# Kernel optimization log

Hardware: AMD Instinct MI355X
Metric: run time of the kernel (lower is better)

Reference implementation:

```python
import jax, jax.numpy as jnp
import numpy as np

B, J, D = 512, 22, 3
HIDDEN = 512
OUT = J * D          # 66, flattened frame size
NCLS = 12
LENGTH = 64


def setup_inputs() -> dict:
    key = jax.random.key(0)
    ks = jax.random.split(key, 12)
    s = 0.05
    return {
        "inputs": jax.random.normal(ks[0], (B, J, D), dtype=jnp.float32),
        "labels": jax.random.randint(ks[1], (B,), 0, NCLS),
        "length": LENGTH,
        # LSTMCell params (torch layout: W_ih [4H, in], W_hh [4H, H], gate order i,f,g,o)
        "W_ih": jax.random.normal(ks[2], (4 * HIDDEN, OUT + NCLS), dtype=jnp.float32) * s,
        "W_hh": jax.random.normal(ks[3], (4 * HIDDEN, HIDDEN), dtype=jnp.float32) * s,
        "b_ih": jax.random.normal(ks[4], (4 * HIDDEN,), dtype=jnp.float32) * s,
        "b_hh": jax.random.normal(ks[5], (4 * HIDDEN,), dtype=jnp.float32) * s,
        # fc: hidden -> output
        "W_fc": jax.random.normal(ks[6], (OUT, HIDDEN), dtype=jnp.float32) * s,
        "b_fc": jax.random.normal(ks[7], (OUT,), dtype=jnp.float32) * s,
        # fc_inh / fc_inc: output -> hidden (initial state projections)
        "W_inh": jax.random.normal(ks[8], (HIDDEN, OUT), dtype=jnp.float32) * s,
        "b_inh": jax.random.normal(ks[9], (HIDDEN,), dtype=jnp.float32) * s,
        "W_inc": jax.random.normal(ks[10], (HIDDEN, OUT), dtype=jnp.float32) * s,
        "b_inc": jax.random.normal(ks[11], (HIDDEN,), dtype=jnp.float32) * s,
    }


def reference(inputs, labels, length, W_ih, W_hh, b_ih, b_hh, W_fc, b_fc,
              W_inh, b_inh, W_inc, b_inc):
    b, j, d = inputs.shape
    enc = jax.nn.one_hot(labels, NCLS, dtype=inputs.dtype)      # [B, NCLS]
    frame0 = inputs.reshape(b, j * d)                            # [B, OUT]
    h0 = frame0 @ W_inh.T + b_inh                                # [B, H]
    c0 = frame0 @ W_inc.T + b_inc                                # [B, H]
    frame = jnp.concatenate([frame0, enc], axis=-1)              # [B, OUT+NCLS]

    def step(carry, _):
        h, c, fr = carry
        gates = fr @ W_ih.T + b_ih + h @ W_hh.T + b_hh           # [B, 4H]
        i, f, g, o = jnp.split(gates, 4, axis=-1)                # torch gate order
        c_new = jax.nn.sigmoid(f) * c + jax.nn.sigmoid(i) * jnp.tanh(g)
        h_new = jax.nn.sigmoid(o) * jnp.tanh(c_new)
        out = h_new @ W_fc.T + b_fc                              # [B, OUT]
        fr_new = jnp.concatenate([out, enc], axis=-1)
        return (h_new, c_new, fr_new), out

    _, outs = jax.lax.scan(step, (h0, c0, frame), None, length=length)  # [L, B, OUT]
    return jnp.transpose(outs, (1, 0, 2)).reshape(b, length, j, d)
```

## Files before the change

### kernel.cpp

```cpp
#include <hip/hip_runtime.h>

#define OUTD 66
#define INW  78
#define FH   2048
#define LEN  64

typedef short bf16x8 __attribute__((ext_vector_type(8)));
typedef float f32x4  __attribute__((ext_vector_type(4)));
typedef unsigned int u32x4 __attribute__((ext_vector_type(4)));

__device__ __forceinline__ float bf2f(unsigned short u) {
  union { unsigned int i; float f; } v; v.i = ((unsigned int)u) << 16; return v.f;
}
__device__ __forceinline__ unsigned short f2bf(float f) {
  union { float f; unsigned int i; } v; v.f = f;
  unsigned int u = v.i;
  return (unsigned short)((u + 0x7fffu + ((u >> 16) & 1u)) >> 16);
}
__device__ __forceinline__ float sigm(float x) { return 1.f / (1.f + __expf(-x)); }
__device__ __forceinline__ float tanh_f(float x) { return 2.f / (1.f + __expf(-2.f * x)) - 1.f; }

__device__ __forceinline__ unsigned int atom_or_ret(unsigned int* p, unsigned int d) {
  unsigned int r;
  asm volatile("global_atomic_or %0, %1, %2, off sc0\n\ts_waitcnt vmcnt(0)"
               : "=&v"(r) : "v"(p), "v"(d) : "memory");
  return r;
}
__device__ __forceinline__ void atom_or(unsigned int* p, unsigned int d) {
  asm volatile("global_atomic_or %0, %1, off" :: "v"(p), "v"(d) : "memory");
}

__global__ __launch_bounds__(256) void k_initA(
    const float* __restrict__ W_hh, const float* __restrict__ W_ih,
    const float* __restrict__ W_fc, const float* __restrict__ b_ih,
    const float* __restrict__ b_hh, const float* __restrict__ b_fc,
    const float* __restrict__ inp, const float* __restrict__ W_inh,
    const float* __restrict__ b_inh, const float* __restrict__ W_inc,
    const float* __restrict__ b_inc,
    unsigned short* __restrict__ Weff, float* __restrict__ bias_eff,
    unsigned short* __restrict__ hbuf, float* __restrict__ c0,
    unsigned short* __restrict__ Wfc16, unsigned int* __restrict__ flags,
    unsigned int* __restrict__ flagsL)
{
  int tid = threadIdx.x, bid = blockIdx.x;
  if (bid < 256) {
    int nb = bid;
    int k = tid * 2;
    float acc[8][2];
    #pragma unroll
    for (int r = 0; r < 8; ++r) {
      int n = nb * 8 + r;
      acc[r][0] = W_hh[n * 512 + k];
      acc[r][1] = W_hh[n * 512 + k + 1];
    }
    for (int m = 0; m < OUTD; ++m) {
      float w0 = W_fc[m * 512 + k];
      float w1 = W_fc[m * 512 + k + 1];
      #pragma unroll
      for (int r = 0; r < 8; ++r) {
        float wih = W_ih[(nb * 8 + r) * INW + m];
        acc[r][0] += wih * w0;
        acc[r][1] += wih * w1;
      }
    }
    #pragma unroll
    for (int r = 0; r < 8; ++r) {
      int n = nb * 8 + r;
      unsigned int pack = (unsigned int)f2bf(acc[r][0]) | ((unsigned int)f2bf(acc[r][1]) << 16);
      *(unsigned int*)(Weff + n * 512 + k) = pack;
    }
    if (tid < 8) {
      int n = nb * 8 + tid;
      float a = b_ih[n] + b_hh[n];
      for (int m = 0; m < OUTD; ++m) a += b_fc[m] * W_ih[n * INW + m];
      bias_eff[n] = a;
    }
    if (nb == 0) {
      for (int i = tid; i < 512 * 16; i += 256) flags[i] = 0;
      for (int i = tid; i < 256 * 16; i += 256) flagsL[i] = 0;
    }
  } else {
    int nb = bid - 256;
    for (int r = 0; r < 2; ++r) {
      int b = nb * 2 + r;
      for (int half = 0; half < 2; ++half) {
        int c = tid + half * 256;
        float ha = b_inh[c], ca = b_inc[c];
        for (int m = 0; m < OUTD; ++m) {
          float f = inp[b * OUTD + m];
          ha += f * W_inh[c * OUTD + m];
          ca += f * W_inc[c * OUTD + m];
        }
        hbuf[((b >> 6) * 32 + (c >> 4)) * 1024 + (b & 63) * 16 + (c & 15)] = f2bf(ha);
        c0[b * 512 + c] = ca;
      }
    }
    if (nb == 0) {
      for (int i = tid; i < OUTD * 512; i += 256) Wfc16[i] = f2bf(W_fc[i]);
    }
  }
}

__global__ __launch_bounds__(128) void k_init2a(
    const float* __restrict__ inp, const unsigned short* __restrict__ hbuf,
    const float* __restrict__ W_fc, const float* __restrict__ b_fc,
    float* __restrict__ d0)
{
  int b = blockIdx.x, m = threadIdx.x;
  if (m >= OUTD) return;
  const unsigned short* hb = hbuf + (b >> 6) * 32768 + (b & 63) * 16;
  const float* wrow = W_fc + m * 512;
  float acc = 0.f;
  for (int k = 0; k < 512; ++k)
    acc += bf2f(hb[(k >> 4) * 1024 + (k & 15)]) * wrow[k];
  d0[b * OUTD + m] = inp[b * OUTD + m] - (acc + b_fc[m]);
}

__global__ __launch_bounds__(256) void k_init2b(
    const float* __restrict__ d0, const float* __restrict__ W_ih,
    float* __restrict__ corr0)
{
  __shared__ float ds[4][OUTD];
  int tid = threadIdx.x, b0 = blockIdx.x * 4;
  for (int i = tid; i < 4 * OUTD; i += 256) ds[i / OUTD][i % OUTD] = d0[b0 * OUTD + i];
  __syncthreads();
  for (int n = tid; n < FH; n += 256) {
    float a0 = 0, a1 = 0, a2 = 0, a3 = 0;
    const float* wr = W_ih + n * INW;
    for (int m = 0; m < OUTD; ++m) {
      float w = wr[m];
      a0 += ds[0][m] * w; a1 += ds[1][m] * w; a2 += ds[2][m] * w; a3 += ds[3][m] * w;
    }
    corr0[(b0 + 0) * FH + n] = a0;
    corr0[(b0 + 1) * FH + n] = a1;
    corr0[(b0 + 2) * FH + n] = a2;
    corr0[(b0 + 3) * FH + n] = a3;
  }
}

__global__ __launch_bounds__(256, 1) void k_main(
    const unsigned short* __restrict__ Weff, const float* __restrict__ bias_eff,
    unsigned short* __restrict__ hbuf, const float* __restrict__ c0,
    const float* __restrict__ corr0, const float* __restrict__ W_ih,
    const int* __restrict__ labels, const unsigned short* __restrict__ Wfc16,
    const float* __restrict__ b_fc, float* __restrict__ out,
    unsigned int* __restrict__ flags, unsigned int* __restrict__ flagsL)
{
  __shared__ __align__(16) unsigned short h_lds[64 * 512];

  int tid = threadIdx.x, bid = blockIdx.x;
  int w = tid >> 6, lane = tid & 63;
  int lc = lane & 15, kg = lane >> 4;
  unsigned int* xmap = flags + 4096;
  unsigned int* decp = flags + 4088;
  unsigned int* maskW = flagsL;

  unsigned int xcd;
  asm volatile("s_getreg_b32 %0, hwreg(HW_REG_XCC_ID)" : "=s"(xcd));
  if (tid == 0)
    __hip_atomic_store(&xmap[bid * 16], xcd + 1u, __ATOMIC_RELAXED, __HIP_MEMORY_SCOPE_AGENT);

  if (bid == 0 && w == 0) {
    int okA = 1, okB = 1;
    #pragma unroll
    for (int i = 0; i < 4; ++i) {
      int b = lane + i * 64;
      unsigned int v, ra, rb;
      const unsigned int* xp = &xmap[b * 16];
      for (;;) { v = __hip_atomic_load(xp, __ATOMIC_RELAXED, __HIP_MEMORY_SCOPE_AGENT);
                 if (v) break; __builtin_amdgcn_s_sleep(1); }
      const unsigned int* pa = &xmap[(b & 7) * 16];
      for (;;) { ra = __hip_atomic_load(pa, __ATOMIC_RELAXED, __HIP_MEMORY_SCOPE_AGENT);
                 if (ra) break; __builtin_amdgcn_s_sleep(1); }
      const unsigned int* pb = &xmap[((b >> 5) << 5) * 16];
      for (;;) { rb = __hip_atomic_load(pb, __ATOMIC_RELAXED, __HIP_MEMORY_SCOPE_AGENT);
                 if (rb) break; __builtin_amdgcn_s_sleep(1); }
      okA &= (v == ra); okB &= (v == rb);
    }
    okA = __all(okA); okB = __all(okB);
    if (lane == 0) {
      unsigned int d = okA ? 1u : (okB ? 2u : 3u);
      __hip_atomic_store(decp, d, __ATOMIC_RELAXED, __HIP_MEMORY_SCOPE_AGENT);
    }
  }
  if (tid == 0) {
    unsigned int dd;
    for (;;) { dd = __hip_atomic_load(decp, __ATOMIC_RELAXED, __HIP_MEMORY_SCOPE_AGENT);
               if (dd) break; __builtin_amdgcn_s_sleep(1); }
    h_lds[0] = (unsigned short)dd;
  }
  __syncthreads();
  unsigned int dmode = h_lds[0];
  __syncthreads();

  int fast, mt, jt;
  if (dmode == 1u)      { fast = 1; mt = bid & 7;  jt = bid >> 3; }
  else if (dmode == 2u) { fast = 1; mt = bid >> 5; jt = bid & 31; }
  else                  { fast = 0; mt = bid & 7;  jt = bid >> 3; }

  int row0 = mt * 64, j0 = jt * 16;
  int hx0 = (w >> 1) * 8;
  int xloc = lc & 7;
  int G = lc >> 3;
  int hcol = j0 + hx0 + xloc;
  int rw0 = (w & 1) * 32;

  int sA = xloc;
  int tA16 = ((kg ^ sA) & 3) << 4;
  int ue64 = ((sA >> 2) & 1) << 6;
  int PA0 = (rw0 + lc) * 1024 + tA16 + ue64;
  int PA1 = PA0 + 16 * 1024;
  int PF  = (w * 16 + lc) * 1024 + tA16 + ue64;

  bf16x8 Bfrag[16][2];
  #pragma unroll
  for (int cg = 0; cg < 2; ++cg) {
    int n = (cg * 2 + G) * 512 + hcol;
    const unsigned short* p = Weff + n * 512 + kg * 8;
    #pragma unroll
    for (int i = 0; i < 16; ++i) Bfrag[i][cg] = *(const bf16x8*)(p + i * 32);
  }

  bf16x8 Wf[16];
  float fcb = 0.f;
  {
    int n = j0 + lc;
    if (jt < 5 && n < OUTD) {
      const unsigned short* p = Wfc16 + n * 512 + kg * 8;
      #pragma unroll
      for (int i = 0; i < 16; ++i) Wf[i] = *(const bf16x8*)(p + i * 32);
      fcb = b_fc[n];
    } else {
      bf16x8 z8 = {0, 0, 0, 0, 0, 0, 0, 0};
      #pragma unroll
      for (int i = 0; i < 16; ++i) Wf[i] = z8;
    }
  }

  int qsel = G * 2;
  float lt[4][4], creg[4];
  #pragma unroll
  for (int idx = 0; idx < 4; ++idx) {
    int rloc = rw0 + (idx >> 1) * 16 + kg * 4 + qsel + (idx & 1);
    int grow = row0 + rloc;
    int lab = labels[grow];
    #pragma unroll
    for (int gt = 0; gt < 4; ++gt) {
      int n = gt * 512 + hcol;
      lt[gt][idx] = bias_eff[n] + W_ih[n * INW + OUTD + lab];
    }
    creg[idx] = c0[grow * 512 + hcol];
  }

  const f32x4 z = {0.f, 0.f, 0.f, 0.f};
  unsigned int* myflag = &flags[(mt * 32 + jt) * 16];

  {
    const unsigned short* hsrc = hbuf + mt * 32768;
    #pragma unroll
    for (int i = 0; i < 16; ++i) {
      int n = tid + i * 256;
      int c = n >> 7, q = n & 127;
      int r = q >> 1, u = q & 1, g = c * 2 + u;
      *(u32x4*)(h_lds + r * 512 + ((g ^ (r & 7)) << 3)) =
          *(const u32x4*)(hsrc + n * 8);
    }
  }
  __syncthreads();

  for (int s = 0; s < LEN; ++s) {
    f32x4 acc00 = z, acc01 = z, acc10 = z, acc11 = z;
    #pragma unroll
    for (int i = 0; i < 16; ++i) {
      bf16x8 a0 = *(const bf16x8*)((const char*)h_lds + (PA0 ^ (i << 6)));
      bf16x8 a1 = *(const bf16x8*)((const char*)h_lds + (PA1 ^ (i << 6)));
      acc00 = __builtin_amdgcn_mfma_f32_16x16x32_bf16(a0, Bfrag[i][0], acc00, 0, 0, 0);
      acc10 = __builtin_amdgcn_mfma_f32_16x16x32_bf16(a1, Bfrag[i][0], acc10, 0, 0, 0);
      acc01 = __builtin_amdgcn_mfma_f32_16x16x32_bf16(a0, Bfrag[i][1], acc01, 0, 0, 0);
      acc11 = __builtin_amdgcn_mfma_f32_16x16x32_bf16(a1, Bfrag[i][1], acc11, 0, 0, 0);
    }

    f32x4 sh00, sh01, sh10, sh11;
    #pragma unroll
    for (int j = 0; j < 4; ++j) {
      sh00[j] = __shfl_xor(acc00[j], 8);
      sh01[j] = __shfl_xor(acc01[j], 8);
      sh10[j] = __shfl_xor(acc10[j], 8);
      sh11[j] = __shfl_xor(acc11[j], 8);
    }

    unsigned short hval[4];
    #pragma unroll
    for (int idx = 0; idx < 4; ++idx) {
      int jj = idx & 1, hh = idx >> 1;
      int qo = qsel + jj;
      float xi, xf, xg, xo;
      if (hh == 0) {
        xi = (G ? sh00[qo] : acc00[qo]);
        xf = (G ? acc00[qo] : sh00[qo]);
        xg = (G ? sh01[qo] : acc01[qo]);
        xo = (G ? acc01[qo] : sh01[qo]);
      } else {
        xi = (G ? sh10[qo] : acc10[qo]);
        xf = (G ? acc10[qo] : sh10[qo]);
        xg = (G ? sh11[qo] : acc11[qo]);
        xo = (G ? acc11[qo] : sh11[qo]);
      }
      xi += lt[0][idx]; xf += lt[1][idx]; xg += lt[2][idx]; xo += lt[3][idx];
      if (s == 0) {
        int rloc = rw0 + hh * 16 + kg * 4 + qo;
        const float* cr = corr0 + (long)(row0 + rloc) * FH + hcol;
        xi += cr[0]; xf += cr[512]; xg += cr[1024]; xo += cr[1536];
      }
      float cn = sigm(xf) * creg[idx] + sigm(xi) * tanh_f(xg);
      creg[idx] = cn;
      hval[idx] = f2bf(sigm(xo) * tanh_f(cn));
    }

    unsigned int pkS[2]; int rlS[2];
    {
      unsigned int* hdst32 = (unsigned int*)(hbuf + ((s + 1) & 1) * 262144);
      int base32 = (mt * 32 + jt) * 512;
      int ceL = (hx0 >> 1) + (xloc >> 1);
      int odd = xloc & 1;
      int np = 0;
      #pragma unroll
      for (int idx = 0; idx < 4; ++idx) {
        unsigned int mine = hval[idx];
        unsigned int part = (unsigned int)__shfl_xor((int)mine, 1);
        unsigned int p = odd ? (part | (mine << 16)) : (mine | (part << 16));
        if ((idx >> 1) == odd) {
          int rloc = rw0 + (idx >> 1) * 16 + kg * 4 + qsel + (idx & 1);
          pkS[np] = p; rlS[np] = rloc; ++np;
        }
      }
      if (fast) {
        hdst32[base32 + rlS[0] * 8 + ceL] = pkS[0];
        hdst32[base32 + rlS[1] * 8 + ceL] = pkS[1];
      } else {
        __hip_atomic_store(&hdst32[base32 + rlS[0] * 8 + ceL], pkS[0],
                           __ATOMIC_RELAXED, __HIP_MEMORY_SCOPE_AGENT);
        __hip_atomic_store(&hdst32[base32 + rlS[1] * 8 + ceL], pkS[1],
                           __ATOMIC_RELAXED, __HIP_MEMORY_SCOPE_AGENT);
      }
    }

    __builtin_amdgcn_s_waitcnt(0);
    __syncthreads();
    if (tid == 0) {
      if (fast)
        atom_or(&maskW[(mt * 4 + (jt >> 3)) * 64 + s], 1u << (jt & 7));
      __hip_atomic_store(myflag, (unsigned int)(s + 1),
                         __ATOMIC_RELAXED, __HIP_MEMORY_SCOPE_AGENT);
    }

    f32x4 fa = z;
    int dofc = (jt < 5) & (s >= 1);
    if (dofc) {
      #pragma unroll
      for (int i = 0; i < 16; ++i) {
        bf16x8 a = *(const bf16x8*)((const char*)h_lds + (PF ^ (i << 6)));
        fa = __builtin_amdgcn_mfma_f32_16x16x32_bf16(a, Wf[i], fa, 0, 0, 0);
      }
    }
    __syncthreads();

    {
      int gS = jt * 2 + (w >> 1);
      unsigned int* l32 = (unsigned int*)h_lds;
      #pragma unroll
      for (int t = 0; t < 2; ++t) {
        int rl = rlS[t];
        l32[rl * 256 + ((gS ^ (rl & 7)) << 2) + (xloc >> 1)] = pkS[t];
      }
    }

    if (s < LEN - 1 || jt < 5) {
      const unsigned short* hbC = hbuf + ((s + 1) & 1) * 262144 + mt * 32768;
      unsigned int mydone = (w == (jt >> 3)) ? (1u << (jt & 7)) : 0u;
      const unsigned int* fA = flags + (mt * 32 + w * 8 + (lane & 7)) * 16;
      unsigned int* mg = &maskW[(mt * 4 + w) * 64 + s];
      int agentMode = !fast;
      int spins = 0;
      while (mydone != 0xffu) {
        unsigned int avail;
        if (!agentMode) {
          unsigned int v = 0;
          if (lane == 0) v = atom_or_ret(mg, 0u);
          avail = (unsigned int)__shfl((int)v, 0);
          if (++spins > 1024) agentMode = 1;
        } else {
          unsigned int fv = __hip_atomic_load(fA, __ATOMIC_RELAXED, __HIP_MEMORY_SCOPE_AGENT);
          avail = (unsigned int)__ballot((int)(fv >= (unsigned int)(s + 1))) & 0xffu;
        }
        unsigned int todo = avail & ~mydone;
        if (!todo) { __builtin_amdgcn_s_sleep(1); continue; }

        if (agentMode)
          __builtin_amdgcn_fence(__ATOMIC_ACQUIRE, "agent");
        else
          asm volatile("buffer_inv\n\ts_waitcnt vmcnt(0)" ::: "memory");

        u32x4 ta[8], tb[8];
        #pragma unroll
        for (int i = 0; i < 8; ++i) {
          if ((todo >> i) & 1u) {
            const unsigned short* cp = hbC + (w * 8 + i) * 1024 + lane * 8;
            ta[i] = *(const u32x4*)cp;
            tb[i] = *(const u32x4*)(cp + 512);
          }
        }
        int r0_ = lane >> 1, u = lane & 1, r1_ = 32 + r0_;
        #pragma unroll
        for (int i = 0; i < 8; ++i) {
          if ((todo >> i) & 1u) {
            int c2 = (w * 8 + i) * 2 + u;
            *(u32x4*)(h_lds + r0_ * 512 + ((c2 ^ (r0_ & 7)) << 3)) = ta[i];
            *(u32x4*)(h_lds + r1_ * 512 + ((c2 ^ (r1_ & 7)) << 3)) = tb[i];
          }
        }
        mydone |= todo;
      }
    }

    if (dofc) {
      int c = j0 + lc;
      if (c < OUTD) {
        #pragma unroll
        for (int q = 0; q < 4; ++q) {
          int b = row0 + w * 16 + kg * 4 + q;
          out[((long)b * 64 + (s - 1)) * OUTD + c] = fa[q] + fcb;
        }
      }
    }
    __syncthreads();
  }

  if (jt < 5) {
    f32x4 fa = z;
    #pragma unroll
    for (int i = 0; i < 16; ++i) {
      bf16x8 a = *(const bf16x8*)((const char*)h_lds + (PF ^ (i << 6)));
      fa = __builtin_amdgcn_mfma_f32_16x16x32_bf16(a, Wf[i], fa, 0, 0, 0);
    }
    int c = j0 + lc;
    if (c < OUTD) {
      #pragma unroll
      for (int q = 0; q < 4; ++q) {
        int b = row0 + w * 16 + kg * 4 + q;
        out[((long)b * 64 + 63) * OUTD + c] = fa[q] + fcb;
      }
    }
  }
}

extern "C" void kernel_launch(void* const* d_in, const int* in_sizes, int n_in,
                              void* d_out, int out_size, void* d_ws, size_t ws_size,
                              hipStream_t stream) {
  (void)in_sizes; (void)n_in; (void)out_size; (void)ws_size;
  const float* inp   = (const float*)d_in[0];
  const int*   labels= (const int*)d_in[1];
  const float* W_ih  = (const float*)d_in[3];
  const float* W_hh  = (const float*)d_in[4];
  const float* b_ih  = (const float*)d_in[5];
  const float* b_hh  = (const float*)d_in[6];
  const float* W_fc  = (const float*)d_in[7];
  const float* b_fc  = (const float*)d_in[8];
  const float* W_inh = (const float*)d_in[9];
  const float* b_inh = (const float*)d_in[10];
  const float* W_inc = (const float*)d_in[11];
  const float* b_inc = (const float*)d_in[12];

  char* ws = (char*)d_ws;
  unsigned short* Weff = (unsigned short*)(ws + 0);
  float* bias_eff      = (float*)(ws + 2097152);
  unsigned short* hbuf = (unsigned short*)(ws + 2105344);
  float* c0            = (float*)(ws + 3153920);
  float* corr0         = (float*)(ws + 4202496);
  float* d0            = (float*)(ws + 8396800);
  unsigned int* flags  = (unsigned int*)(ws + 8531968);
  unsigned short* Wfc16= (unsigned short*)(ws + 8564736);
  unsigned int* flagsL = (unsigned int*)(ws + 8632320);

  k_initA<<<512, 256, 0, stream>>>(W_hh, W_ih, W_fc, b_ih, b_hh, b_fc,
                                   inp, W_inh, b_inh, W_inc, b_inc,
                                   Weff, bias_eff, hbuf, c0, Wfc16, flags, flagsL);
  k_init2a<<<512, 128, 0, stream>>>(inp, hbuf, W_fc, b_fc, d0);
  k_init2b<<<128, 256, 0, stream>>>(d0, W_ih, corr0);

  k_main<<<256, 256, 0, stream>>>(Weff, bias_eff, hbuf, c0, corr0, W_ih, labels,
                                  Wfc16, b_fc, (float*)d_out, flags, flagsL);
}
```

Baseline: 450.8 us.

## Split persistent LSTM kernel into 512 blocks with 32-row batch tiles

Halves the batch rows per block from 64 to 32 and doubles the persistent grid to 512 blocks with two blocks per CU, rearranging the hidden-state buffer layout, flag strides and XCD mapping to match. Each block now does half the MFMA work per step, and the FC output store is deferred into the next step to overlap with compute. This gives more parallelism per step but doubles the number of blocks taking part in the cross-block flag synchronisation, and it relies on all 512 blocks being co-resident.

```diff
diff --git a/kernel.cpp b/kernel.cpp
--- a/kernel.cpp
+++ b/kernel.cpp
@@ -91,7 +91,7 @@
           ha += f * W_inh[c * OUTD + m];
           ca += f * W_inc[c * OUTD + m];
         }
-        hbuf[((b >> 6) * 32 + (c >> 4)) * 1024 + (b & 63) * 16 + (c & 15)] = f2bf(ha);
+        hbuf[((b >> 5) * 32 + (c >> 4)) * 512 + (b & 31) * 16 + (c & 15)] = f2bf(ha);
         c0[b * 512 + c] = ca;
       }
     }
@@ -108,11 +108,11 @@
 {
   int b = blockIdx.x, m = threadIdx.x;
   if (m >= OUTD) return;
-  const unsigned short* hb = hbuf + (b >> 6) * 32768 + (b & 63) * 16;
+  const unsigned short* hb = hbuf + (b >> 5) * 16384 + (b & 31) * 16;
   const float* wrow = W_fc + m * 512;
   float acc = 0.f;
   for (int k = 0; k < 512; ++k)
-    acc += bf2f(hb[(k >> 4) * 1024 + (k & 15)]) * wrow[k];
+    acc += bf2f(hb[(k >> 4) * 512 + (k & 15)]) * wrow[k];
   d0[b * OUTD + m] = inp[b * OUTD + m] - (acc + b_fc[m]);
 }
 
@@ -138,7 +138,7 @@
   }
 }
 
-__global__ __launch_bounds__(256, 1) void k_main(
+__global__ __launch_bounds__(256, 2) void k_main(
     const unsigned short* __restrict__ Weff, const float* __restrict__ bias_eff,
     unsigned short* __restrict__ hbuf, const float* __restrict__ c0,
     const float* __restrict__ corr0, const float* __restrict__ W_ih,
@@ -146,33 +146,33 @@
     const float* __restrict__ b_fc, float* __restrict__ out,
     unsigned int* __restrict__ flags, unsigned int* __restrict__ flagsL)
 {
-  __shared__ __align__(16) unsigned short h_lds[64 * 512];
+  __shared__ __align__(16) unsigned short h_lds[32 * 512];
 
   int tid = threadIdx.x, bid = blockIdx.x;
   int w = tid >> 6, lane = tid & 63;
   int lc = lane & 15, kg = lane >> 4;
-  unsigned int* xmap = flags + 4096;
-  unsigned int* decp = flags + 4088;
+  unsigned int* xmap = flags + 4608;
+  unsigned int* decp = flags + 4100;
   unsigned int* maskW = flagsL;
 
   unsigned int xcd;
   asm volatile("s_getreg_b32 %0, hwreg(HW_REG_XCC_ID)" : "=s"(xcd));
   if (tid == 0)
-    __hip_atomic_store(&xmap[bid * 16], xcd + 1u, __ATOMIC_RELAXED, __HIP_MEMORY_SCOPE_AGENT);
+    __hip_atomic_store(&xmap[bid * 4], xcd + 1u, __ATOMIC_RELAXED, __HIP_MEMORY_SCOPE_AGENT);
 
   if (bid == 0 && w == 0) {
     int okA = 1, okB = 1;
     #pragma unroll
-    for (int i = 0; i < 4; ++i) {
+    for (int i = 0; i < 8; ++i) {
       int b = lane + i * 64;
       unsigned int v, ra, rb;
-      const unsigned int* xp = &xmap[b * 16];
+      const unsigned int* xp = &xmap[b * 4];
       for (;;) { v = __hip_atomic_load(xp, __ATOMIC_RELAXED, __HIP_MEMORY_SCOPE_AGENT);
                  if (v) break; __builtin_amdgcn_s_sleep(1); }
-      const unsigned int* pa = &xmap[(b & 7) * 16];
+      const unsigned int* pa = &xmap[(b & 15) * 4];
       for (;;) { ra = __hip_atomic_load(pa, __ATOMIC_RELAXED, __HIP_MEMORY_SCOPE_AGENT);
                  if (ra) break; __builtin_amdgcn_s_sleep(1); }
-      const unsigned int* pb = &xmap[((b >> 5) << 5) * 16];
+      const unsigned int* pb = &xmap[((b >> 5) << 5) * 4];
       for (;;) { rb = __hip_atomic_load(pb, __ATOMIC_RELAXED, __HIP_MEMORY_SCOPE_AGENT);
                  if (rb) break; __builtin_amdgcn_s_sleep(1); }
       okA &= (v == ra); okB &= (v == rb);
@@ -194,23 +194,22 @@
   __syncthreads();
 
   int fast, mt, jt;
-  if (dmode == 1u)      { fast = 1; mt = bid & 7;  jt = bid >> 3; }
-  else if (dmode == 2u) { fast = 1; mt = bid >> 5; jt = bid & 31; }
-  else                  { fast = 0; mt = bid & 7;  jt = bid >> 3; }
-
-  int row0 = mt * 64, j0 = jt * 16;
+  if (dmode == 1u)      { fast = 1; mt = bid & 15;  jt = bid >> 4; }
+  else if (dmode == 2u) { fast = 1; mt = bid >> 5;  jt = bid & 31; }
+  else                  { fast = 0; mt = bid & 15;  jt = bid >> 4; }
+
+  int row0 = mt * 32, j0 = jt * 16;
   int hx0 = (w >> 1) * 8;
   int xloc = lc & 7;
   int G = lc >> 3;
   int hcol = j0 + hx0 + xloc;
-  int rw0 = (w & 1) * 32;
+  int rw0 = (w & 1) * 16;
 
   int sA = xloc;
   int tA16 = ((kg ^ sA) & 3) << 4;
   int ue64 = ((sA >> 2) & 1) << 6;
   int PA0 = (rw0 + lc) * 1024 + tA16 + ue64;
-  int PA1 = PA0 + 16 * 1024;
-  int PF  = (w * 16 + lc) * 1024 + tA16 + ue64;
+  int PF  = ((w & 1) * 16 + lc) * 1024 + tA16 + ue64;
 
   bf16x8 Bfrag[16][2];
   #pragma unroll
@@ -225,7 +224,7 @@
   float fcb = 0.f;
   {
     int n = j0 + lc;
-    if (jt < 5 && n < OUTD) {
+    if (jt < 5 && w < 2 && n < OUTD) {
       const unsigned short* p = Wfc16 + n * 512 + kg * 8;
       #pragma unroll
       for (int i = 0; i < 16; ++i) Wf[i] = *(const bf16x8*)(p + i * 32);
@@ -238,10 +237,10 @@
   }
 
   int qsel = G * 2;
-  float lt[4][4], creg[4];
+  float lt[4][2], creg[2];
   #pragma unroll
-  for (int idx = 0; idx < 4; ++idx) {
-    int rloc = rw0 + (idx >> 1) * 16 + kg * 4 + qsel + (idx & 1);
+  for (int idx = 0; idx < 2; ++idx) {
+    int rloc = rw0 + kg * 4 + qsel + idx;
     int grow = row0 + rloc;
     int lab = labels[grow];
     #pragma unroll
@@ -253,14 +252,14 @@
   }
 
   const f32x4 z = {0.f, 0.f, 0.f, 0.f};
-  unsigned int* myflag = &flags[(mt * 32 + jt) * 16];
+  unsigned int* myflag = &flags[(mt * 32 + jt) * 8];
 
   {
-    const unsigned short* hsrc = hbuf + mt * 32768;
-    #pragma unroll
-    for (int i = 0; i < 16; ++i) {
+    const unsigned short* hsrc = hbuf + mt * 16384;
+    #pragma unroll
+    for (int i = 0; i < 8; ++i) {
       int n = tid + i * 256;
-      int c = n >> 7, q = n & 127;
+      int c = n >> 6, q = n & 63;
       int r = q >> 1, u = q & 1, g = c * 2 + u;
       *(u32x4*)(h_lds + r * 512 + ((g ^ (r & 7)) << 3)) =
           *(const u32x4*)(hsrc + n * 8);
@@ -268,47 +267,48 @@
   }
   __syncthreads();
 
+  f32x4 faP = z; int havP = 0, colP = 0;
+  int dofcW = (jt < 5) & (w < 2);
+
   for (int s = 0; s < LEN; ++s) {
-    f32x4 acc00 = z, acc01 = z, acc10 = z, acc11 = z;
+    if (havP) {
+      int c = j0 + lc;
+      if (c < OUTD) {
+        #pragma unroll
+        for (int q = 0; q < 4; ++q) {
+          int b = row0 + (w & 1) * 16 + kg * 4 + q;
+          out[((long)b * 64 + colP) * OUTD + c] = faP[q] + fcb;
+        }
+      }
+      havP = 0;
+    }
+
+    f32x4 acc00 = z, acc01 = z;
     #pragma unroll
     for (int i = 0; i < 16; ++i) {
       bf16x8 a0 = *(const bf16x8*)((const char*)h_lds + (PA0 ^ (i << 6)));
-      bf16x8 a1 = *(const bf16x8*)((const char*)h_lds + (PA1 ^ (i << 6)));
       acc00 = __builtin_amdgcn_mfma_f32_16x16x32_bf16(a0, Bfrag[i][0], acc00, 0, 0, 0);
-      acc10 = __builtin_amdgcn_mfma_f32_16x16x32_bf16(a1, Bfrag[i][0], acc10, 0, 0, 0);
       acc01 = __builtin_amdgcn_mfma_f32_16x16x32_bf16(a0, Bfrag[i][1], acc01, 0, 0, 0);
-      acc11 = __builtin_amdgcn_mfma_f32_16x16x32_bf16(a1, Bfrag[i][1], acc11, 0, 0, 0);
-    }
-
-    f32x4 sh00, sh01, sh10, sh11;
+    }
+
+    f32x4 sh00, sh01;
     #pragma unroll
     for (int j = 0; j < 4; ++j) {
       sh00[j] = __shfl_xor(acc00[j], 8);
       sh01[j] = __shfl_xor(acc01[j], 8);
-      sh10[j] = __shfl_xor(acc10[j], 8);
-      sh11[j] = __shfl_xor(acc11[j], 8);
-    }
-
-    unsigned short hval[4];
-    #pragma unroll
-    for (int idx = 0; idx < 4; ++idx) {
-      int jj = idx & 1, hh = idx >> 1;
-      int qo = qsel + jj;
-      float xi, xf, xg, xo;
-      if (hh == 0) {
-        xi = (G ? sh00[qo] : acc00[qo]);
-        xf = (G ? acc00[qo] : sh00[qo]);
-        xg = (G ? sh01[qo] : acc01[qo]);
-        xo = (G ? acc01[qo] : sh01[qo]);
-      } else {
-        xi = (G ? sh10[qo] : acc10[qo]);
-        xf = (G ? acc10[qo] : sh10[qo]);
-        xg = (G ? sh11[qo] : acc11[qo]);
-        xo = (G ? acc11[qo] : sh11[qo]);
-      }
+    }
+
+    unsigned short hval[2];
+    #pragma unroll
+    for (int idx = 0; idx < 2; ++idx) {
+      int qo = qsel + idx;
+      float xi = (G ? sh00[qo] : acc00[qo]);
+      float xf = (G ? acc00[qo] : sh00[qo]);
+      float xg = (G ? sh01[qo] : acc01[qo]);
+      float xo = (G ? acc01[qo] : sh01[qo]);
       xi += lt[0][idx]; xf += lt[1][idx]; xg += lt[2][idx]; xo += lt[3][idx];
       if (s == 0) {
-        int rloc = rw0 + hh * 16 + kg * 4 + qo;
+        int rloc = rw0 + kg * 4 + qo;
         const float* cr = corr0 + (long)(row0 + rloc) * FH + hcol;
         xi += cr[0]; xf += cr[512]; xg += cr[1024]; xo += cr[1536];
       }
@@ -317,30 +317,23 @@
       hval[idx] = f2bf(sigm(xo) * tanh_f(cn));
     }
 
-    unsigned int pkS[2]; int rlS[2];
+    unsigned int pkS = 0; int rlS = 0;
     {
       unsigned int* hdst32 = (unsigned int*)(hbuf + ((s + 1) & 1) * 262144);
-      int base32 = (mt * 32 + jt) * 512;
+      int base32 = (mt * 32 + jt) * 256;
       int ceL = (hx0 >> 1) + (xloc >> 1);
       int odd = xloc & 1;
-      int np = 0;
-      #pragma unroll
-      for (int idx = 0; idx < 4; ++idx) {
+      #pragma unroll
+      for (int idx = 0; idx < 2; ++idx) {
         unsigned int mine = hval[idx];
         unsigned int part = (unsigned int)__shfl_xor((int)mine, 1);
         unsigned int p = odd ? (part | (mine << 16)) : (mine | (part << 16));
-        if ((idx >> 1) == odd) {
-          int rloc = rw0 + (idx >> 1) * 16 + kg * 4 + qsel + (idx & 1);
-          pkS[np] = p; rlS[np] = rloc; ++np;
-        }
+        if (idx == odd) { pkS = p; rlS = rw0 + kg * 4 + qsel + idx; }
       }
       if (fast) {
-        hdst32[base32 + rlS[0] * 8 + ceL] = pkS[0];
-        hdst32[base32 + rlS[1] * 8 + ceL] = pkS[1];
+        hdst32[base32 + rlS * 8 + ceL] = pkS;
       } else {
-        __hip_atomic_store(&hdst32[base32 + rlS[0] * 8 + ceL], pkS[0],
-                           __ATOMIC_RELAXED, __HIP_MEMORY_SCOPE_AGENT);
-        __hip_atomic_store(&hdst32[base32 + rlS[1] * 8 + ceL], pkS[1],
+        __hip_atomic_store(&hdst32[base32 + rlS * 8 + ceL], pkS,
                            __ATOMIC_RELAXED, __HIP_MEMORY_SCOPE_AGENT);
       }
     }
@@ -354,31 +347,28 @@
                          __ATOMIC_RELAXED, __HIP_MEMORY_SCOPE_AGENT);
     }
 
-    f32x4 fa = z;
-    int dofc = (jt < 5) & (s >= 1);
+    int dofc = dofcW & (s >= 1);
     if (dofc) {
+      f32x4 fa = z;
       #pragma unroll
       for (int i = 0; i < 16; ++i) {
         bf16x8 a = *(const bf16x8*)((const char*)h_lds + (PF ^ (i << 6)));
         fa = __builtin_amdgcn_mfma_f32_16x16x32_bf16(a, Wf[i], fa, 0, 0, 0);
       }
+      faP = fa; havP = 1; colP = s - 1;
     }
     __syncthreads();
 
     {
       int gS = jt * 2 + (w >> 1);
       unsigned int* l32 = (unsigned int*)h_lds;
-      #pragma unroll
-      for (int t = 0; t < 2; ++t) {
-        int rl = rlS[t];
-        l32[rl * 256 + ((gS ^ (rl & 7)) << 2) + (xloc >> 1)] = pkS[t];
-      }
+      l32[rlS * 256 + ((gS ^ (rlS & 7)) << 2) + (xloc >> 1)] = pkS;
     }
 
     if (s < LEN - 1 || jt < 5) {
-      const unsigned short* hbC = hbuf + ((s + 1) & 1) * 262144 + mt * 32768;
+      const unsigned short* hbC = hbuf + ((s + 1) & 1) * 262144 + mt * 16384;
       unsigned int mydone = (w == (jt >> 3)) ? (1u << (jt & 7)) : 0u;
-      const unsigned int* fA = flags + (mt * 32 + w * 8 + (lane & 7)) * 16;
+      const unsigned int* fA = flags + (mt * 32 + w * 8 + (lane & 7)) * 8;
       unsigned int* mg = &maskW[(mt * 4 + w) * 64 + s];
       int agentMode = !fast;
       int spins = 0;
@@ -401,53 +391,47 @@
         else
           asm volatile("buffer_inv\n\ts_waitcnt vmcnt(0)" ::: "memory");
 
-        u32x4 ta[8], tb[8];
+        u32x4 ta[8];
         #pragma unroll
         for (int i = 0; i < 8; ++i) {
           if ((todo >> i) & 1u) {
-            const unsigned short* cp = hbC + (w * 8 + i) * 1024 + lane * 8;
+            const unsigned short* cp = hbC + (w * 8 + i) * 512 + lane * 8;
             ta[i] = *(const u32x4*)cp;
-            tb[i] = *(const u32x4*)(cp + 512);
           }
         }
-        int r0_ = lane >> 1, u = lane & 1, r1_ = 32 + r0_;
+        int r_ = lane >> 1, u = lane & 1;
         #pragma unroll
         for (int i = 0; i < 8; ++i) {
           if ((todo >> i) & 1u) {
             int c2 = (w * 8 + i) * 2 + u;
-            *(u32x4*)(h_lds + r0_ * 512 + ((c2 ^ (r0_ & 7)) << 3)) = ta[i];
-            *(u32x4*)(h_lds + r1_ * 512 + ((c2 ^ (r1_ & 7)) << 3)) = tb[i];
+            *(u32x4*)(h_lds + r_ * 512 + ((c2 ^ (r_ & 7)) << 3)) = ta[i];
           }
         }
         mydone |= todo;
       }
     }
-
-    if (dofc) {
-      int c = j0 + lc;
-      if (c < OUTD) {
-        #pragma unroll
-        for (int q = 0; q < 4; ++q) {
-          int b = row0 + w * 16 + kg * 4 + q;
-          out[((long)b * 64 + (s - 1)) * OUTD + c] = fa[q] + fcb;
-        }
-      }
-    }
     __syncthreads();
   }
 
-  if (jt < 5) {
+  if (dofcW) {
+    int c = j0 + lc;
+    if (havP && c < OUTD) {
+      #pragma unroll
+      for (int q = 0; q < 4; ++q) {
+        int b = row0 + (w & 1) * 16 + kg * 4 + q;
+        out[((long)b * 64 + colP) * OUTD + c] = faP[q] + fcb;
+      }
+    }
     f32x4 fa = z;
     #pragma unroll
     for (int i = 0; i < 16; ++i) {
       bf16x8 a = *(const bf16x8*)((const char*)h_lds + (PF ^ (i << 6)));
       fa = __builtin_amdgcn_mfma_f32_16x16x32_bf16(a, Wf[i], fa, 0, 0, 0);
     }
-    int c = j0 + lc;
     if (c < OUTD) {
       #pragma unroll
       for (int q = 0; q < 4; ++q) {
-        int b = row0 + w * 16 + kg * 4 + q;
+        int b = row0 + (w & 1) * 16 + kg * 4 + q;
         out[((long)b * 64 + 63) * OUTD + c] = fa[q] + fcb;
       }
     }
@@ -488,6 +472,6 @@
   k_init2a<<<512, 128, 0, stream>>>(inp, hbuf, W_fc, b_fc, d0);
   k_init2b<<<128, 256, 0, stream>>>(d0, W_ih, corr0);
 
-  k_main<<<256, 256, 0, stream>>>(Weff, bias_eff, hbuf, c0, corr0, W_ih, labels,
+  k_main<<<512, 256, 0, stream>>>(Weff, bias_eff, hbuf, c0, corr0, W_ih, labels,
                                   Wfc16, b_fc, (float*)d_out, flags, flagsL);
 }
```

New measurement: 464.9 us. +3.1%, slower.
